# Kernel tuning notes

Measured on AMD Instinct MI355X. Metric: run time of the kernel, lower is better.

The kernel has to match this reference:

```python
import jax, jax.numpy as jnp
from jax import lax
import numpy as np

# Module config (from init_kwargs)
NUM_SEG_ROW = 8
NUM_SEG_COL = 8
H = 224
W = 224
K = NUM_SEG_ROW * NUM_SEG_COL  # 64 labels
B = 4


def setup_inputs() -> dict:
    key = jax.random.key(0)
    grad_map = jax.random.normal(key, (B, 1, H, W), dtype=jnp.float32)
    return {"grad_map": grad_map, "band_width": 5, "num_iterations": 5}


def _dp_paths(neg_g):
    """Dynamic-programming min-cost path. neg_g: (L, P, M) per-step costs.
    Returns positions (L, P): index in [0, M) chosen at each step."""
    L, P, M = neg_g.shape
    m = jnp.arange(M)
    # clamp(m + {-1,0,1}, 0, M-1); torch's inf padding is never hit after clamping
    nbr = jnp.clip(m[:, None] + jnp.array([-1, 0, 1])[None, :], 0, M - 1)  # (M,3)

    def step(prev_cost, g_row):
        pc = prev_cost[:, nbr]                      # (P, M, 3)
        amin = pc.argmin(axis=2)                    # (P, M)
        min_prev = jnp.take_along_axis(pc, amin[..., None], axis=2)[..., 0]
        path_row = nbr[m[None, :], amin]            # (P, M) predecessor position
        new_cost = min_prev + g_row
        return new_cost, (new_cost, path_row)

    _, (costs, paths) = lax.scan(step, neg_g[0], neg_g[1:])  # paths: (L-1, P, M)
    idx_last = costs[-1].argmin(axis=1)             # (P,)

    def back(idx, path_row):
        new_idx = path_row[jnp.arange(path_row.shape[0]), idx]
        return new_idx, idx

    first_idx, pos_tail = lax.scan(back, idx_last, paths, reverse=True)
    positions = jnp.concatenate([first_idx[None], pos_tail], axis=0)  # (L, P)
    return positions


def _boundary_masks(grad2d, x_inits, y_inits, band_width):
    """grad2d: (H, W). Returns (vmask, hmask) boolean (H, W)."""
    offs = jnp.arange(-band_width, band_width + 1)
    P = x_inits.shape[0]
    # vertical paths (one x per row)
    x_idx = jnp.clip(x_inits[:, None] + offs[None, :], 0, W - 1)   # (P, M)
    pos_v = _dp_paths(-grad2d[:, x_idx])                            # (H, P)
    coords_v = x_idx[jnp.arange(P)[None, :], pos_v]                 # (H, P) x-coords
    vmask = jnp.zeros((H, W), bool).at[jnp.arange(H)[:, None], coords_v].set(True)
    # horizontal paths (one y per column)
    y_idx = jnp.clip(y_inits[:, None] + offs[None, :], 0, H - 1)    # (P, M)
    pos_h = _dp_paths(-grad2d.T[:, y_idx])                          # (W, P)
    coords_h = y_idx[jnp.arange(P)[None, :], pos_h]                 # (W, P) y-coords
    hmask = jnp.zeros((H, W), bool).at[coords_h, jnp.arange(W)[:, None]].set(True)
    return vmask, hmask


def _one_hot_nchw(labels):
    return jax.nn.one_hot(labels, K, dtype=jnp.float32).transpose(0, 3, 1, 2)


def _box_vote(oh, ksize):
    # grouped (depthwise) conv with all-ones kernel == neighborhood vote count
    kern = jnp.ones((K, 1, ksize, ksize), oh.dtype)
    pad = ksize // 2
    return lax.conv_general_dilated(
        oh, kern, window_strides=(1, 1), padding=[(pad, pad), (pad, pad)],
        dimension_numbers=("NCHW", "OIHW", "NCHW"), feature_group_count=K)


def reference(grad_map, band_width, num_iterations):
    x_inits = jnp.clip(jnp.array([i * (W // NUM_SEG_COL) for i in range(1, NUM_SEG_COL)]), 0, W - 1)
    y_inits = jnp.clip(jnp.array([i * (H // NUM_SEG_ROW) for i in range(1, NUM_SEG_ROW)]), 0, H - 1)
    vmask, hmask = jax.vmap(lambda g: _boundary_masks(g, x_inits, y_inits, band_width))(grad_map[:, 0])
    v_labels = jnp.cumsum(vmask.astype(jnp.int32), axis=2)
    h_labels = jnp.cumsum(hmask.astype(jnp.int32), axis=1)
    seg = v_labels + NUM_SEG_COL * h_labels                         # (B, H, W), values in [0, K)
    # multi-scale connectivity voting
    oh = _one_hot_nchw(seg)
    labels = seg
    for _ in range(num_iterations):
        vote_sum = _box_vote(oh, 3) + _box_vote(oh, 5) + _box_vote(oh, 7)
        labels = vote_sum.argmax(axis=1)
        oh = _one_hot_nchw(labels)
    return labels
```

## Files before the change

### kernel.cpp

```cpp
#include <hip/hip_runtime.h>
#include <stdint.h>

#define HH 224
#define WW 224
#define BB 4
#define PP 7
#define SEG 28
#define BW 5
#define MM 11

#define POS_INF_I 0x7F800000

typedef const __attribute__((address_space(1))) unsigned int* gas_ptr;
typedef __attribute__((address_space(3))) unsigned int* las_ptr;
typedef unsigned long long ull;

__device__ inline ull mcompose(ull F, ull G) {
    ull H = 0ull;
#pragma unroll
    for (int i = 0; i < 11; ++i) {
        unsigned g = (unsigned)(G >> (4 * i)) & 15u;
        H |= ((F >> (4 * g)) & 15ull) << (4 * i);
    }
    return H;
}

__device__ __forceinline__ void tile_map(int& bx, int& by, int& b) {
    int p = blockIdx.x;
    int v = (p & 7) * 98 + (p >> 3);
    bx = v % 14;
    int r = v / 14;
    by = r % 14;
    b  = r / 14;
}

__device__ __forceinline__ void lane_map(int t, int& tx, int& ty) {
    const int lane = t & 63;
    const int w    = t >> 6;
    tx = ((w & 1) << 3) + (lane & 7);
    ty = ((w >> 1) << 3) + (lane >> 3);
}

__global__ __launch_bounds__(64) void dp_kernel(const float* __restrict__ grad,
                                                int* __restrict__ coords_v,
                                                int* __restrict__ coords_h) {
    __shared__ __align__(16) float gseg[225 * 16];

    const int tid = threadIdx.x;
    const int l   = tid & 15;
    const int sid = blockIdx.x;
    const int p   = sid % PP;
    const int dir = (sid / PP) & 1;
    const int b   = sid / (2 * PP);
    const int base = SEG * (p + 1);
    const float* gb = grad + b * (HH * WW);

    {
        const int r  = tid >> 4;
        const int m  = tid & 15;
        const int sS = (dir == 0) ? WW : 1;
        const int sM = (dir == 0) ? 1  : WW;
        const float* src = gb + r * sS + (base - BW + m) * sM;
        const long stepBytes = (long)(4 * sS) * 4;
#pragma unroll 8
        for (int c = 0; c < 56; ++c) {
            __builtin_amdgcn_global_load_lds((gas_ptr)(const void*)src,
                                             (las_ptr)(void*)(&gseg[c * 64]), 4, 0, 0);
            src = (const float*)((const char*)src + stepBytes);
        }
    }
    __syncthreads();

    const float lane_add = (l < MM) ? 0.0f : __int_as_float(POS_INF_I);
    const float* gp = &gseg[l];

    unsigned wreg[16] = {};

#define DP_STEP(gval, ownb, jj_c)                                                       \
    {                                                                                   \
        float v1 = cost;                                                                \
        float v0 = __int_as_float(__builtin_amdgcn_update_dpp(                          \
            POS_INF_I, __float_as_int(cost), 0x111, 0xf, 0xf, false));                  \
        float v2 = __int_as_float(__builtin_amdgcn_update_dpp(                          \
            POS_INF_I, __float_as_int(cost), 0x101, 0xf, 0xf, false));                  \
        bool a01 = (v0 <= v1), a02 = (v0 <= v2), a12 = (v1 <= v2);                      \
        bool aa  = a01 && a02;                                                          \
        unsigned long long A   = __ballot(aa);                                          \
        unsigned long long C12 = __ballot(a12);                                         \
        unsigned long long B0 = ~A & C12;                                               \
        unsigned long long B1 = ~A & ~C12;                                              \
        float mv = aa ? v0 : (a12 ? v1 : v2);                                           \
        cost = mv - (gval) + lane_add;                                                  \
        unsigned wv = (unsigned)(B0 & 0x7FFull) | ((unsigned)(B1 & 0x7FFull) << 11);    \
        wreg[(jj_c)] = (ownb) ? wv : wreg[(jj_c)];                                      \
    }

    float cost = -gp[0] + lane_add;
    float buf[16], c0[16];
#pragma unroll
    for (int k = 0; k < 16; ++k) buf[k] = gp[(1 + k) * 16];
    for (int t = 0; t < 13; ++t) {
        const bool own = (tid == t);
#pragma unroll
        for (int k = 0; k < 16; ++k) c0[k] = buf[k];
#pragma unroll
        for (int k = 0; k < 16; ++k) buf[k] = gp[(16 * (t + 1) + 1 + k) * 16];
#pragma unroll
        for (int k = 0; k < 16; ++k) DP_STEP(c0[k], own, k)
    }
    {
        const bool own = (tid == 13);
#pragma unroll
        for (int k = 0; k < 15; ++k) DP_STEP(buf[k], own, k)
    }
#undef DP_STEP

    float bc = cost;
    int   bi = l;
#pragma unroll
    for (int mask = 1; mask < 16; mask <<= 1) {
        float oc = __shfl_xor(bc, mask, 16);
        int   oi = __shfl_xor(bi, mask, 16);
        if (oc < bc || (oc == bc && oi < bi)) { bc = oc; bi = oi; }
    }
    const int idx_last = bi;

    const int mcnt = (l < 13) ? 16 : ((l == 13) ? 15 : 0);
    const ull IDMAP = 0xA9876543210ull;
    ull L = IDMAP;
#pragma unroll
    for (int jj = 15; jj >= 0; --jj) {
        if (jj < mcnt) {
            unsigned ww = wreg[jj];
            ull M = 0ull;
#pragma unroll
            for (int i = 0; i < MM; ++i) {
                unsigned sel = ((ww >> i) & 1u) + 2u * ((ww >> (11 + i)) & 1u);
                M |= ((ull)(i + (int)sel - 1)) << (4 * i);
            }
            L = mcompose(M, L);
        }
    }
    ull I = L;
#pragma unroll
    for (int d = 1; d < 16; d <<= 1) {
        ull O = __shfl_down(I, d, 16);
        if (l + d < 16) I = mcompose(I, O);
    }
    ull R = __shfl_down(I, 1, 16);
    if (l == 15) R = IDMAP;

    int* cout = (dir == 0) ? coords_v : coords_h;
    if (tid == 15) cout[(b * HH + 223) * PP + p] = base + idx_last - BW;
    if (tid < 16) {
        unsigned v = (unsigned)(R >> (4 * idx_last)) & 15u;
#pragma unroll
        for (int jj = 15; jj >= 0; --jj) {
            if (jj < mcnt) {
                unsigned ww = wreg[jj];
                unsigned sel = ((ww >> v) & 1u) + 2u * ((ww >> (11 + v)) & 1u);
                v = v + sel - 1u;
                cout[(b * HH + (16 * l + jj)) * PP + p] = base + (int)v - BW;
            }
        }
    }
}

#define RW 22
#define RH 22
#define RSTR 24

__global__ __launch_bounds__(256) void labvote_kernel(const int* __restrict__ cv,
                                                      const int* __restrict__ ch,
                                                      unsigned char* __restrict__ out8) {
    __shared__ unsigned char lab[RH * RSTR];
    __shared__ unsigned bins[16 * 256];
    const int t = threadIdx.x;
    int tx, ty;
    lane_map(t, tx, ty);
    int bxt, byt, b;
    tile_map(bxt, byt, b);
    const int GX0 = bxt * 16, GY0 = byt * 16;

    for (int idx = t; idx < RW * RH; idx += 256) {
        int j = idx / RW, i = idx - j * RW;
        int gx = GX0 - 3 + i, gy = GY0 - 3 + j;
        if ((unsigned)gx < WW && (unsigned)gy < HH) {
            const int* cvp = cv + (b * HH + gy) * PP;
            const int* chp = ch + (b * WW + gx) * PP;
            int v = 0, h = 0;
#pragma unroll
            for (int q = 0; q < PP; ++q) { v += (cvp[q] <= gx); h += (chp[q] <= gy); }
            lab[j * RSTR + i] = (unsigned char)(v + 8 * h);
        }
    }
    __syncthreads();

    const int gx = GX0 + tx, gy = GY0 + ty;
#pragma unroll
    for (int c = 0; c < 16; ++c) bins[c * 256 + t] = 0u;
#pragma unroll
    for (int dy = -3; dy <= 3; ++dy) {
        if ((unsigned)(gy + dy) >= HH) continue;
#pragma unroll
        for (int dx = -3; dx <= 3; ++dx) {
            if ((unsigned)(gx + dx) >= WW) continue;
            int lb = lab[(ty + 3 + dy) * RSTR + (tx + 3 + dx)];
            int ay = dy < 0 ? -dy : dy, ax = dx < 0 ? -dx : dx;
            int d = ay > ax ? ay : ax;
            unsigned wgt = (d <= 1) ? 3u : (unsigned)(4 - d);
            atomicAdd(&bins[(lb >> 2) * 256 + t], wgt << ((lb & 3) * 8));
        }
    }
    int best_s = 0, best_k = 0;
#pragma unroll
    for (int c = 0; c < 16; ++c) {
        unsigned wd = bins[c * 256 + t];
        if (wd) {
#pragma unroll
            for (int q = 0; q < 4; ++q) {
                int s = (int)((wd >> (q * 8)) & 255u);
                if (s > best_s) { best_s = s; best_k = c * 4 + q; }
            }
        }
    }
    out8[(b * HH + gy) * WW + gx] = (unsigned char)best_k;
}

__global__ __launch_bounds__(256) void vote_kernel(const unsigned char* __restrict__ in,
                                                   unsigned char* __restrict__ out8,
                                                   int* __restrict__ out32) {
    __shared__ unsigned bins[16 * 256];
    const int t = threadIdx.x;
    int tx, ty;
    lane_map(t, tx, ty);
    int bxt, byt, b;
    tile_map(bxt, byt, b);
    const int x = bxt * 16 + tx;
    const int y = byt * 16 + ty;
    const unsigned char* img = in + b * (HH * WW);

    ull rows[7];
    const bool xedge = (bxt == 0) || (bxt == 13);
    if (!xedge) {
        const unsigned* img32 = (const unsigned*)img;
        const int o0 = x - 3;
#pragma unroll
        for (int dy = -3; dy <= 3; ++dy) {
            int yc = min(max(y + dy, 0), HH - 1);
            int o  = yc * WW + o0;
            int a  = o >> 2;
            int sh = (o & 3) * 8;
            unsigned d0 = img32[a], d1 = img32[a + 1], d2 = img32[a + 2];
            ull lo = ((ull)d1 << 32) | d0;
            ull row = lo >> sh;
            if (sh) row |= (ull)d2 << (64 - sh);
            rows[dy + 3] = row & 0x00FFFFFFFFFFFFFFull;
        }
    } else {
#pragma unroll
        for (int dy = -3; dy <= 3; ++dy) {
            int yc = min(max(y + dy, 0), HH - 1);
            ull row = 0ull;
#pragma unroll
            for (int dx = -3; dx <= 3; ++dx) {
                int xc = min(max(x + dx, 0), WW - 1);
                row |= (ull)img[yc * WW + xc] << (8 * (dx + 3));
            }
            rows[dy + 3] = row;
        }
    }

    const unsigned labc = (unsigned)((rows[3] >> 24) & 255u);
    const ull rep = (ull)labc * 0x0001010101010101ull;
    bool uni = true;
#pragma unroll
    for (int k = 0; k < 7; ++k) uni = uni && (rows[k] == rep);

    int best_k;
    if (uni) {
        best_k = (int)labc;
    } else {
#pragma unroll
        for (int c = 0; c < 16; ++c) bins[c * 256 + t] = 0u;
#pragma unroll
        for (int dy = -3; dy <= 3; ++dy) {
            if ((unsigned)(y + dy) >= (unsigned)HH) continue;
            ull row = rows[dy + 3];
            const int ay = dy < 0 ? -dy : dy;
#pragma unroll
            for (int dx = -3; dx <= 3; ++dx) {
                if ((unsigned)(x + dx) >= (unsigned)WW) continue;
                int lb = (int)((row >> (8 * (dx + 3))) & 255u);
                const int ax = dx < 0 ? -dx : dx;
                const int d = ay > ax ? ay : ax;
                const unsigned wgt = (d <= 1) ? 3u : (unsigned)(4 - d);
                atomicAdd(&bins[(lb >> 2) * 256 + t], wgt << ((lb & 3) * 8));
            }
        }
        int best_s = 0; best_k = 0;
#pragma unroll
        for (int c = 0; c < 16; ++c) {
            unsigned wd = bins[c * 256 + t];
            if (wd) {
#pragma unroll
                for (int q = 0; q < 4; ++q) {
                    int s = (int)((wd >> (q * 8)) & 255u);
                    if (s > best_s) { best_s = s; best_k = c * 4 + q; }
                }
            }
        }
    }

    int o = (b * HH + y) * WW + x;
    if (out8)  out8[o]  = (unsigned char)best_k;
    if (out32) out32[o] = best_k;
}

extern "C" void kernel_launch(void* const* d_in, const int* in_sizes, int n_in,
                              void* d_out, int out_size, void* d_ws, size_t ws_size,
                              hipStream_t stream) {
    (void)in_sizes; (void)n_in; (void)out_size; (void)ws_size;
    const float* grad = (const float*)d_in[0];
    int* out = (int*)d_out;
    char* ws = (char*)d_ws;

    int* cv = (int*)(ws);
    int* ch = (int*)(ws + 25088);
    unsigned char* laW = (unsigned char*)(ws + 50176);
    unsigned char* laD = (unsigned char*)d_out;

    dp_kernel<<<56, 64, 0, stream>>>(grad, cv, ch);

    dim3 grid(784, 1, 1), blk(256, 1, 1);
    labvote_kernel<<<grid, blk, 0, stream>>>(cv, ch, laD);
    vote_kernel<<<grid, blk, 0, stream>>>(laD, laW, nullptr);
    vote_kernel<<<grid, blk, 0, stream>>>(laW, laD, nullptr);
    vote_kernel<<<grid, blk, 0, stream>>>(laD, laW, nullptr);
    vote_kernel<<<grid, blk, 0, stream>>>(laW, nullptr, out);
}
```

Before: 111.6 us.

## Fuse pairs of voting iterations into single kernels using shared-memory halo recompute

Consecutive vote iterations are fused into one kernel: each block computes a 28x28 label tile with a 6-pixel halo in LDS, votes a 22x22 intermediate region, then votes the final 16x16 tile. This cuts the launches from five to three and removes the global round trips between fused iterations. The cost is redundant halo recomputation of the intermediate region (484 versus 256 pixels) and extra syncthreads. Out-of-image halo pixels are clamped to edge labels, and the bounds checks inside the vote use the clamped coordinates.

```diff
diff --git a/kernel.cpp b/kernel.cpp
--- a/kernel.cpp
+++ b/kernel.cpp
@@ -14,6 +14,10 @@
 typedef const __attribute__((address_space(1))) unsigned int* gas_ptr;
 typedef __attribute__((address_space(3))) unsigned int* las_ptr;
 typedef unsigned long long ull;
+
+__device__ __forceinline__ int iclamp(int v, int lo, int hi) {
+    return min(max(v, lo), hi);
+}
 
 __device__ inline ull mcompose(ull F, ull G) {
     ull H = 0ull;
@@ -166,49 +170,22 @@
     }
 }
 
-#define RW 22
-#define RH 22
-#define RSTR 24
-
-__global__ __launch_bounds__(256) void labvote_kernel(const int* __restrict__ cv,
-                                                      const int* __restrict__ ch,
-                                                      unsigned char* __restrict__ out8) {
-    __shared__ unsigned char lab[RH * RSTR];
-    __shared__ unsigned bins[16 * 256];
-    const int t = threadIdx.x;
-    int tx, ty;
-    lane_map(t, tx, ty);
-    int bxt, byt, b;
-    tile_map(bxt, byt, b);
-    const int GX0 = bxt * 16, GY0 = byt * 16;
-
-    for (int idx = t; idx < RW * RH; idx += 256) {
-        int j = idx / RW, i = idx - j * RW;
-        int gx = GX0 - 3 + i, gy = GY0 - 3 + j;
-        if ((unsigned)gx < WW && (unsigned)gy < HH) {
-            const int* cvp = cv + (b * HH + gy) * PP;
-            const int* chp = ch + (b * WW + gx) * PP;
-            int v = 0, h = 0;
-#pragma unroll
-            for (int q = 0; q < PP; ++q) { v += (cvp[q] <= gx); h += (chp[q] <= gy); }
-            lab[j * RSTR + i] = (unsigned char)(v + 8 * h);
-        }
-    }
-    __syncthreads();
-
-    const int gx = GX0 + tx, gy = GY0 + ty;
+__device__ __forceinline__ int slow_vote_bins(const ull* rows, int x, int y, int t,
+                                              unsigned* __restrict__ bins) {
 #pragma unroll
     for (int c = 0; c < 16; ++c) bins[c * 256 + t] = 0u;
 #pragma unroll
     for (int dy = -3; dy <= 3; ++dy) {
-        if ((unsigned)(gy + dy) >= HH) continue;
+        if ((unsigned)(y + dy) >= (unsigned)HH) continue;
+        ull row = rows[dy + 3];
+        const int ay = dy < 0 ? -dy : dy;
 #pragma unroll
         for (int dx = -3; dx <= 3; ++dx) {
-            if ((unsigned)(gx + dx) >= WW) continue;
-            int lb = lab[(ty + 3 + dy) * RSTR + (tx + 3 + dx)];
-            int ay = dy < 0 ? -dy : dy, ax = dx < 0 ? -dx : dx;
-            int d = ay > ax ? ay : ax;
-            unsigned wgt = (d <= 1) ? 3u : (unsigned)(4 - d);
+            if ((unsigned)(x + dx) >= (unsigned)WW) continue;
+            int lb = (int)((row >> (8 * (dx + 3))) & 255u);
+            const int ax = dx < 0 ? -dx : dx;
+            const int d = ay > ax ? ay : ax;
+            const unsigned wgt = (d <= 1) ? 3u : (unsigned)(4 - d);
             atomicAdd(&bins[(lb >> 2) * 256 + t], wgt << ((lb & 3) * 8));
         }
     }
@@ -224,18 +201,140 @@
             }
         }
     }
-    out8[(b * HH + gy) * WW + gx] = (unsigned char)best_k;
+    return best_k;
+}
+
+template<int STR>
+__device__ __forceinline__ void gather7(const unsigned char* lab,
+                                        int cx0, int cy0, ull* rows) {
+#pragma unroll
+    for (int r = 0; r < 7; ++r) {
+        int o  = (cy0 + r) * STR + cx0;
+        int a8 = o & ~7;
+        int sh = (o & 7) * 8;
+        ull lo = *reinterpret_cast<const ull*>(lab + a8);
+        ull hi = *reinterpret_cast<const ull*>(lab + a8 + 8);
+        ull row = lo >> sh;
+        if (sh) row |= hi << (64 - sh);
+        rows[r] = row & 0x00FFFFFFFFFFFFFFull;
+    }
+}
+
+__device__ __forceinline__ int do_vote(const ull* rows, int x, int y, int t,
+                                       unsigned* __restrict__ bins) {
+    const unsigned cl = (unsigned)((rows[3] >> 24) & 255u);
+    const ull rep = (ull)cl * 0x0001010101010101ull;
+    bool uni = true;
+#pragma unroll
+    for (int k = 0; k < 7; ++k) uni = uni && (rows[k] == rep);
+    if (uni) return (int)cl;
+    return slow_vote_bins(rows, x, y, t, bins);
+}
+
+__global__ __launch_bounds__(256) void labvote12_kernel(const int* __restrict__ cv,
+                                                        const int* __restrict__ ch,
+                                                        unsigned char* __restrict__ out8) {
+    __shared__ int cvs[28 * PP];
+    __shared__ int chs[28 * PP];
+    __shared__ __align__(8) unsigned char labL[28 * 32];
+    __shared__ __align__(8) unsigned char labM[22 * 24];
+    __shared__ unsigned bins[16 * 256];
+
+    const int t = threadIdx.x;
+    int tx, ty;  lane_map(t, tx, ty);
+    int bxt, byt, b;  tile_map(bxt, byt, b);
+    const int GX0 = bxt * 16, GY0 = byt * 16;
+
+    for (int idx = t; idx < 28 * PP; idx += 256) {
+        int gyc = iclamp(GY0 - 6 + idx / PP, 0, HH - 1);
+        cvs[idx] = cv[(b * HH + gyc) * PP + idx % PP];
+    }
+    for (int idx = t; idx < 28 * PP; idx += 256) {
+        int gxc = iclamp(GX0 - 6 + idx / PP, 0, WW - 1);
+        chs[idx] = ch[(b * WW + gxc) * PP + idx % PP];
+    }
+    __syncthreads();
+
+    for (int idx = t; idx < 28 * 28; idx += 256) {
+        int j = idx / 28, i = idx - j * 28;
+        int gxc = iclamp(GX0 - 6 + i, 0, WW - 1);
+        int gyc = iclamp(GY0 - 6 + j, 0, HH - 1);
+        int v = 0, h = 0;
+#pragma unroll
+        for (int q = 0; q < PP; ++q) {
+            v += (cvs[j * PP + q] <= gxc);
+            h += (chs[i * PP + q] <= gyc);
+        }
+        labL[j * 32 + i] = (unsigned char)(v + 8 * h);
+    }
+    __syncthreads();
+
+    for (int idx = t; idx < 22 * 22; idx += 256) {
+        int j = idx / 22, i = idx - j * 22;
+        int gxc = iclamp(GX0 - 3 + i, 0, WW - 1);
+        int gyc = iclamp(GY0 - 3 + j, 0, HH - 1);
+        int cx0 = gxc - GX0 + 3;
+        int cy0 = gyc - GY0 + 3;
+        ull rows[7];
+        gather7<32>(labL, cx0, cy0, rows);
+        labM[j * 24 + i] = (unsigned char)do_vote(rows, gxc, gyc, t, bins);
+    }
+    __syncthreads();
+
+    {
+        const int x = GX0 + tx, y = GY0 + ty;
+        ull rows[7];
+        gather7<24>(labM, tx, ty, rows);
+        out8[(b * HH + y) * WW + x] = (unsigned char)do_vote(rows, x, y, t, bins);
+    }
+}
+
+__global__ __launch_bounds__(256) void vote34_kernel(const unsigned char* __restrict__ in,
+                                                     unsigned char* __restrict__ out8) {
+    __shared__ __align__(8) unsigned char labL[28 * 32];
+    __shared__ __align__(8) unsigned char labM[22 * 24];
+    __shared__ unsigned bins[16 * 256];
+
+    const int t = threadIdx.x;
+    int tx, ty;  lane_map(t, tx, ty);
+    int bxt, byt, b;  tile_map(bxt, byt, b);
+    const int GX0 = bxt * 16, GY0 = byt * 16;
+    const unsigned char* img = in + b * (HH * WW);
+
+    for (int idx = t; idx < 28 * 28; idx += 256) {
+        int j = idx / 28, i = idx - j * 28;
+        int gxc = iclamp(GX0 - 6 + i, 0, WW - 1);
+        int gyc = iclamp(GY0 - 6 + j, 0, HH - 1);
+        labL[j * 32 + i] = img[gyc * WW + gxc];
+    }
+    __syncthreads();
+
+    for (int idx = t; idx < 22 * 22; idx += 256) {
+        int j = idx / 22, i = idx - j * 22;
+        int gxc = iclamp(GX0 - 3 + i, 0, WW - 1);
+        int gyc = iclamp(GY0 - 3 + j, 0, HH - 1);
+        int cx0 = gxc - GX0 + 3;
+        int cy0 = gyc - GY0 + 3;
+        ull rows[7];
+        gather7<32>(labL, cx0, cy0, rows);
+        labM[j * 24 + i] = (unsigned char)do_vote(rows, gxc, gyc, t, bins);
+    }
+    __syncthreads();
+
+    {
+        const int x = GX0 + tx, y = GY0 + ty;
+        ull rows[7];
+        gather7<24>(labM, tx, ty, rows);
+        out8[(b * HH + y) * WW + x] = (unsigned char)do_vote(rows, x, y, t, bins);
+    }
 }
 
 __global__ __launch_bounds__(256) void vote_kernel(const unsigned char* __restrict__ in,
-                                                   unsigned char* __restrict__ out8,
                                                    int* __restrict__ out32) {
     __shared__ unsigned bins[16 * 256];
     const int t = threadIdx.x;
-    int tx, ty;
-    lane_map(t, tx, ty);
-    int bxt, byt, b;
-    tile_map(bxt, byt, b);
+    int tx, ty;  lane_map(t, tx, ty);
+    int bxt, byt, b;  tile_map(bxt, byt, b);
     const int x = bxt * 16 + tx;
     const int y = byt * 16 + ty;
     const unsigned char* img = in + b * (HH * WW);
@@ -271,50 +370,7 @@
         }
     }
 
-    const unsigned labc = (unsigned)((rows[3] >> 24) & 255u);
-    const ull rep = (ull)labc * 0x0001010101010101ull;
-    bool uni = true;
-#pragma unroll
-    for (int k = 0; k < 7; ++k) uni = uni && (rows[k] == rep);
-
-    int best_k;
-    if (uni) {
-        best_k = (int)labc;
-    } else {
-#pragma unroll
-        for (int c = 0; c < 16; ++c) bins[c * 256 + t] = 0u;
-#pragma unroll
-        for (int dy = -3; dy <= 3; ++dy) {
-            if ((unsigned)(y + dy) >= (unsigned)HH) continue;
-            ull row = rows[dy + 3];
-            const int ay = dy < 0 ? -dy : dy;
-#pragma unroll
-            for (int dx = -3; dx <= 3; ++dx) {
-                if ((unsigned)(x + dx) >= (unsigned)WW) continue;
-                int lb = (int)((row >> (8 * (dx + 3))) & 255u);
-                const int ax = dx < 0 ? -dx : dx;
-                const int d = ay > ax ? ay : ax;
-                const unsigned wgt = (d <= 1) ? 3u : (unsigned)(4 - d);
-                atomicAdd(&bins[(lb >> 2) * 256 + t], wgt << ((lb & 3) * 8));
-            }
-        }
-        int best_s = 0; best_k = 0;
-#pragma unroll
-        for (int c = 0; c < 16; ++c) {
-            unsigned wd = bins[c * 256 + t];
-            if (wd) {
-#pragma unroll
-                for (int q = 0; q < 4; ++q) {
-                    int s = (int)((wd >> (q * 8)) & 255u);
-                    if (s > best_s) { best_s = s; best_k = c * 4 + q; }
-                }
-            }
-        }
-    }
-
-    int o = (b * HH + y) * WW + x;
-    if (out8)  out8[o]  = (unsigned char)best_k;
-    if (out32) out32[o] = best_k;
+    out32[(b * HH + y) * WW + x] = do_vote(rows, x, y, t, bins);
 }
 
 extern "C" void kernel_launch(void* const* d_in, const int* in_sizes, int n_in,
@@ -333,9 +389,7 @@
     dp_kernel<<<56, 64, 0, stream>>>(grad, cv, ch);
 
     dim3 grid(784, 1, 1), blk(256, 1, 1);
-    labvote_kernel<<<grid, blk, 0, stream>>>(cv, ch, laD);
-    vote_kernel<<<grid, blk, 0, stream>>>(laD, laW, nullptr);
-    vote_kernel<<<grid, blk, 0, stream>>>(laW, laD, nullptr);
-    vote_kernel<<<grid, blk, 0, stream>>>(laD, laW, nullptr);
-    vote_kernel<<<grid, blk, 0, stream>>>(laW, nullptr, out);
-}
+    labvote12_kernel<<<grid, blk, 0, stream>>>(cv, ch, laD);
+    vote34_kernel<<<grid, blk, 0, stream>>>(laD, laW);
+    vote_kernel<<<grid, blk, 0, stream>>>(laW, out);
+}
```

Result: slower. 114.2 us (+2.3%).
